# Kernel optimization log

Measured on AMD Instinct MI355X. Metric: run time of the kernel, lower is better.

The kernel has to match this reference:

```python
import jax, jax.numpy as jnp
import numpy as np

MAX_SAMPLE = 1024
THRESHOLD = 100
FEAT_W = 0.1
MASK_W = 0.1
TEMP = 0.1
BASE_TEMP = 0.07
IGNORE = 255
EPS = 1e-16


def _l2norm(x, axis):
    # F.normalize: x / max(||x||, 1e-12)
    return x / jnp.maximum(jnp.linalg.norm(x, axis=axis, keepdims=True), 1e-12)


def _mine(predict, label, prob):
    """Host-side hard-sample mining (data-dependent shapes, matches torch loop).
    predict, label: np [B,N]; prob: np [B,N,cls]. Returns (batch_idx, pixel_idx) or None."""
    B = label.shape[0]
    cls_lists, total = [], 0
    for i in range(B):
        vals, counts = np.unique(label[i], return_counts=True)
        per = [int(v) for v, c in zip(vals, counts) if v != IGNORE and c > THRESHOLD]
        cls_lists.append(per)
        total += len(per)
    if total == 0:
        return None
    n_view = min(MAX_SAMPLE // total, THRESHOLD)
    b_list, p_list = [], []
    for i in range(B):
        for c in cls_lists[i]:
            is_c = label[i] == c
            hard = np.nonzero(is_c & (predict[i] != c))[0]
            easy = np.nonzero(is_c & (predict[i] == c))[0]
            nh, ne = hard.shape[0], easy.shape[0]
            if nh >= n_view / 2 and ne >= n_view / 2:
                nhk = n_view // 2
                nek = n_view - nhk
            elif nh >= n_view / 2:
                nek = ne
                nhk = n_view - nek
            elif ne >= n_view / 2:
                nhk = nh
                nek = n_view - nhk
            else:
                nhk = nh
                nek = ne
            hard = hard[np.argsort(-prob[i, hard, c])[:nhk]]  # descending by prob
            easy = easy[np.argsort(prob[i, easy, c])[:nek]]   # ascending by prob
            idx = np.concatenate([hard, easy])
            b_list.append(np.full(idx.shape[0], i, dtype=np.int64))
            p_list.append(idx.astype(np.int64))
    return np.concatenate(b_list), np.concatenate(p_list)


def _feat_contrastive(feature, label):
    n = feature.shape[0]
    logits = feature @ feature.T / TEMP                              # [n,n]
    logits = logits - jax.lax.stop_gradient(jnp.max(logits, axis=1, keepdims=True))
    off_diag = ~jnp.eye(n, dtype=bool)
    pos = ((label[:, None] == label[None, :]) & off_diag).astype(logits.dtype)
    exp_logits = jnp.exp(logits) * off_diag
    log_prob = logits - jnp.log(exp_logits.sum(1, keepdims=True) + EPS)
    mlpp = (pos * log_prob).sum(1) / (pos.sum(1) + EPS)
    return (-(TEMP / BASE_TEMP) * mlpp).mean() * FEAT_W


def _mask_contrastive(anchors, keys, label):
    n, k, c = keys.shape
    all_keys = jnp.concatenate([anchors, keys.reshape(n * k, c)], axis=0)  # [n*(k+1),c]
    same = label[:, None] == label[None, :]
    key_label = jnp.tile(same, (1, k))  # matches torch .repeat(1, repeat_num)
    off_diag = ~jnp.eye(n, dtype=bool)
    tot = jnp.concatenate([same & off_diag, key_label], axis=1)
    neg = (~tot).astype(jnp.float32)
    tot = tot.astype(jnp.float32)
    logits = jnp.einsum('nc,mc->nm', jax.lax.stop_gradient(anchors), all_keys) / TEMP
    logits = logits - jax.lax.stop_gradient(jnp.max(logits, axis=1, keepdims=True))
    log_prob = logits - jnp.log((jnp.exp(logits) * neg).sum(1, keepdims=True) + EPS)
    mlp = (tot * log_prob).sum(1) / (tot.sum(1) + EPS)
    return (-(TEMP / BASE_TEMP) * mlp).mean() * MASK_W


def setup_inputs() -> dict:
    key = jax.random.key(0)
    k1, k2, k3, k4 = jax.random.split(key, 4)
    B, C, H, W = 2, 256, 160, 160
    NCLS, NM, CM = 19, 3, 256
    return {
        'proj_feats': jax.random.normal(k1, (B, C, H, W), jnp.float32),
        'seg_logits': jax.random.normal(k2, (B, NCLS, H, W), jnp.float32),
        'groundtruth': jax.random.randint(k3, (B, 1, H, W), 0, NCLS, dtype=jnp.int32),
        'proj_masks': jax.random.normal(k4, (NM, B, CM, H, W), jnp.float32),
    }


def reference(proj_feats, seg_logits, groundtruth, proj_masks):
    B, C, H, W = proj_feats.shape
    N = H * W
    # groundtruth already at [H,W] -> nearest interp is identity; bilinear same-size is identity.
    label = groundtruth.reshape(B, N)
    prob = jax.nn.softmax(seg_logits, axis=1).reshape(B, -1, N).transpose(0, 2, 1)  # [B,N,cls]
    predict = jnp.argmax(prob, axis=2)                                              # [B,N]
    feats = _l2norm(proj_feats.reshape(B, C, N), 1).transpose(0, 2, 1)              # [B,N,C]
    masks = _l2norm(proj_masks, 2).reshape(proj_masks.shape[0], B, -1, N).transpose(0, 1, 3, 2)  # [M,B,N,Cm]
    mined = _mine(np.asarray(predict), np.asarray(label), np.asarray(prob))
    if mined is None:
        return jnp.stack([proj_feats.mean() * 0, proj_masks.mean() * 0])
    b_idx, p_idx = mined
    sel_feat = feats[b_idx, p_idx]                           # [n,C]
    sel_label = label[b_idx, p_idx]                          # [n]
    sel_anchor = masks[-1][b_idx, p_idx]                     # [n,Cm]
    sel_keys = masks[:-1][:, b_idx, p_idx].transpose(1, 0, 2)  # [n,K,Cm]
    loss_feat = _feat_contrastive(sel_feat, sel_label)
    loss_mask = _mask_contrastive(sel_anchor, sel_keys, sel_label)
    return jnp.stack([loss_feat, loss_mask])
```

## Files before the change

kernel.cpp:

```cpp
#include <hip/hip_runtime.h>
#include <hip/hip_bf16.h>
#include <math.h>

#define B_ 2
#define NCLS_ 19
#define N_ 25600
#define C_ 256
#define MAXN_ 1024
#define THRESH_ 100
#define MAXSAMP_ 1024
#define NLIST_ (B_*NCLS_*2)
#define NHIST_ (B_*NCLS_)
#define NBLK_ 200
#define CAP_ 6144
#define CAPL_ 25600
#define NRF_ 32
#define NRM_ 96

typedef __attribute__((ext_vector_type(8))) short bf16x8;
typedef __attribute__((ext_vector_type(4))) float f32x4;

constexpr size_t OFF_CURS = 0;
constexpr size_t OFF_SELB = 512;
constexpr size_t OFF_SELP = OFF_SELB + (size_t)MAXN_*4;
constexpr size_t OFF_SELL = OFF_SELP + (size_t)MAXN_*4;
constexpr size_t OFF_SFH  = OFF_SELL + (size_t)MAXN_*4;
constexpr size_t OFF_KMH  = OFF_SFH + (size_t)MAXN_*C_*2;
constexpr size_t OFF_PAF  = OFF_KMH + (size_t)3*MAXN_*C_*2;
constexpr size_t OFF_PAM  = OFF_PAF + (size_t)MAXN_*4;
constexpr size_t OFF_PFP  = OFF_PAM + (size_t)MAXN_*4;
constexpr size_t OFF_PMP  = OFF_PFP + (size_t)MAXN_*NRF_*16;
constexpr size_t OFF_CAND = OFF_PMP + (size_t)MAXN_*NRM_*16;

__device__ __forceinline__ unsigned short f2bf(float x) {
    unsigned u = __float_as_uint(x);
    unsigned r = (u + 0x7FFFu + ((u >> 16) & 1u)) >> 16;
    return (unsigned short)r;
}

__device__ __forceinline__ void plan_takes(int ne, int nh, int n_view, int* h, int* e) {
    int nhk, nek;
    bool hb = 2*nh >= n_view, eb = 2*ne >= n_view;
    if (hb && eb)      { nhk = n_view/2; nek = n_view - nhk; }
    else if (hb)       { nek = ne;       nhk = n_view - nek; }
    else if (eb)       { nhk = nh;       nek = n_view - nhk; }
    else               { nhk = nh;       nek = ne; }
    *h = nhk < nh ? nhk : nh;
    *e = nek < ne ? nek : ne;
}

__device__ __forceinline__ int plan_total_n(const int* __restrict__ cursor, int* o_total) {
    int total = 0;
    for (int i = 0; i < NHIST_; ++i)
        if (cursor[2*i] + cursor[2*i+1] > THRESH_) total++;
    int n_view = 0;
    if (total > 0) { n_view = MAXSAMP_ / total; if (n_view > THRESH_) n_view = THRESH_; }
    int off = 0;
    for (int i = 0; i < NHIST_; ++i) {
        int ne = cursor[2*i], nh = cursor[2*i+1];
        if (ne + nh > THRESH_) { int h, e; plan_takes(ne, nh, n_view, &h, &e); off += h + e; }
    }
    if (o_total) *o_total = total;
    return off;
}

__device__ __forceinline__ void plan_slot(const int* __restrict__ cursor, int slot,
                                          int* h_take, int* e_take, int* off_out) {
    int total = 0;
    for (int i = 0; i < NHIST_; ++i)
        if (cursor[2*i] + cursor[2*i+1] > THRESH_) total++;
    int n_view = 0;
    if (total > 0) { n_view = MAXSAMP_ / total; if (n_view > THRESH_) n_view = THRESH_; }
    int off = 0, ht = 0, et = 0, myoff = 0;
    for (int i = 0; i < NHIST_; ++i) {
        int ne = cursor[2*i], nh = cursor[2*i+1];
        int h = 0, e = 0;
        if (ne + nh > THRESH_) plan_takes(ne, nh, n_view, &h, &e);
        if (i == slot) { ht = h; et = e; myoff = off; }
        off += h + e;
    }
    *h_take = ht; *e_take = et; *off_out = myoff;
}

__global__ void __launch_bounds__(256, 2)
k_softmax_scatter(const float* __restrict__ seg, const int* __restrict__ gt,
                  int* __restrict__ cursor, unsigned long long* __restrict__ cand) {
    __shared__ int lcnt[NLIST_];
    __shared__ int lbeg[NLIST_];
    int t = threadIdx.x;
    if (t < NLIST_) lcnt[t] = 0;
    __syncthreads();
    int idx = blockIdx.x * 256 + t;
    int L = -1, lp = 0;
    unsigned long long key = 0;
    if (idx < B_*N_) {
        int b = idx / N_, p = idx - b*N_;
        int lab = gt[idx];
        if (lab >= 0 && lab < NCLS_) {
            const float* base = seg + (size_t)b*NCLS_*N_ + p;
            float v[NCLS_];
            float mx = -INFINITY; int am = 0;
            #pragma unroll
            for (int k = 0; k < NCLS_; ++k) {
                float x = base[(size_t)k*N_];
                v[k] = x;
                if (x > mx) { mx = x; am = k; }
            }
            float ssum = 0.f, pv = 0.f;
            #pragma unroll
            for (int k = 0; k < NCLS_; ++k) {
                float e = expf(v[k] - mx);
                ssum += e;
                pv = (lab == k) ? e : pv;
            }
            pv /= ssum;
            int ishard = (am != lab) ? 1 : 0;
            L = (b*NCLS_ + lab)*2 + ishard;
            lp = atomicAdd(&lcnt[L], 1);
            unsigned int pb = __float_as_uint(pv);
            unsigned int lo = ishard ? (0xFFFFFFFFu - (unsigned int)p) : (unsigned int)p;
            key = ((unsigned long long)pb << 32) | (unsigned long long)lo;
        }
    }
    __syncthreads();
    if (t < NLIST_ && lcnt[t] > 0) lbeg[t] = atomicAdd(&cursor[t], lcnt[t]);
    __syncthreads();
    if (L >= 0) cand[(size_t)L*CAPL_ + lbeg[L] + lp] = key;
}

__global__ void __launch_bounds__(256, 2)
k_select2(const int* __restrict__ cursor, const unsigned long long* __restrict__ cand,
          int* __restrict__ sel_b, int* __restrict__ sel_p, int* __restrict__ sel_l) {
    __shared__ unsigned long long keys[CAP_];
    __shared__ unsigned long long wpart[2][4];
    int bid = blockIdx.x;
    int slot = bid >> 1, ishard = bid & 1;
    int h_take, e_take, base_off;
    plan_slot(cursor, slot, &h_take, &e_take, &base_off);
    int take = ishard ? h_take : e_take;
    if (take == 0) return;
    int off = base_off + (ishard ? 0 : h_take);
    int m = cursor[2*slot + ishard];
    const unsigned long long* g = cand + (size_t)(2*slot + ishard)*CAPL_;
    int t = threadIdx.x, lane = t & 63, w = t >> 6;
    bool fits = (m <= CAP_);
    if (fits) {
        for (int j = t; j < m; j += 256) keys[j] = g[j];
        __syncthreads();
    }
    int b = slot / NCLS_, c = slot - b*NCLS_;
    unsigned long long prev = ishard ? 0xFFFFFFFFFFFFFFFFull : 0ull;
    for (int it = 0; it < take; ++it) {
        unsigned long long best = ishard ? 0ull : 0xFFFFFFFFFFFFFFFFull;
        if (ishard) {
            for (int j = t; j < m; j += 256) {
                unsigned long long k = fits ? keys[j] : g[j];
                if (k < prev && k > best) best = k;
            }
        } else {
            for (int j = t; j < m; j += 256) {
                unsigned long long k = fits ? keys[j] : g[j];
                if (k > prev && k < best) best = k;
            }
        }
        #pragma unroll
        for (int d = 1; d < 64; d <<= 1) {
            unsigned long long o = __shfl_xor(best, d);
            if (ishard ? (o > best) : (o < best)) best = o;
        }
        if (lane == 0) wpart[it & 1][w] = best;
        __syncthreads();
        unsigned long long b0 = wpart[it & 1][0], b1 = wpart[it & 1][1];
        unsigned long long b2 = wpart[it & 1][2], b3 = wpart[it & 1][3];
        if (ishard) {
            unsigned long long hi01 = b0 > b1 ? b0 : b1;
            unsigned long long hi23 = b2 > b3 ? b2 : b3;
            prev = hi01 > hi23 ? hi01 : hi23;
        } else {
            unsigned long long lo01 = b0 < b1 ? b0 : b1;
            unsigned long long lo23 = b2 < b3 ? b2 : b3;
            prev = lo01 < lo23 ? lo01 : lo23;
        }
        if (t == 0) {
            unsigned int lo = (unsigned int)(prev & 0xFFFFFFFFull);
            int p = ishard ? (int)(0xFFFFFFFFu - lo) : (int)lo;
            sel_b[off+it] = b; sel_p[off+it] = p; sel_l[off+it] = c;
        }
    }
}

__global__ void __launch_bounds__(64)
k_gather(const float* __restrict__ pf, const float* __restrict__ pm,
         const int* __restrict__ cursor, const int* __restrict__ sel_b,
         const int* __restrict__ sel_p,
         unsigned short* __restrict__ sfh, unsigned short* __restrict__ km) {
    int bid = blockIdx.x;
    int s = bid >> 2, vec = bid & 3;
    int n = plan_total_n(cursor, nullptr);
    if (s >= n) return;
    int b = sel_b[s], p = sel_p[s];
    int lane = threadIdx.x;
    const float* src;
    unsigned short* dst;
    if (vec == 0)      { src = pf + (size_t)(b*C_)*N_ + p;          dst = sfh + (size_t)s*C_; }
    else if (vec == 1) { src = pm + (size_t)((2*B_+b)*C_)*N_ + p;   dst = km + (size_t)s*C_; }
    else if (vec == 2) { src = pm + (size_t)((0*B_+b)*C_)*N_ + p;   dst = km + (size_t)(n + 2*s)*C_; }
    else               { src = pm + (size_t)((1*B_+b)*C_)*N_ + p;   dst = km + (size_t)(n + 2*s + 1)*C_; }
    float x[4]; float ss = 0.f;
    #pragma unroll
    for (int q = 0; q < 4; ++q) { x[q] = src[(size_t)(lane + 64*q)*N_]; ss += x[q]*x[q]; }
    #pragma unroll
    for (int d = 1; d < 64; d <<= 1) ss += __shfl_xor(ss, d);
    float inv = 1.f / fmaxf(sqrtf(ss), 1e-12f);
    #pragma unroll
    for (int q = 0; q < 4; ++q) dst[lane + 64*q] = f2bf(x[q] * inv);
}

__global__ void __launch_bounds__(256, 4)
k_rows_mfma(const int* __restrict__ cursor, const unsigned short* __restrict__ sfh,
            const unsigned short* __restrict__ km, const int* __restrict__ sel_l,
            float4* __restrict__ pfp, float4* __restrict__ pmp) {
    const int n = plan_total_n(cursor, nullptr);
    const bool maskmode = (blockIdx.y >= 16);
    const int yb = maskmode ? (blockIdx.y - 16) : blockIdx.y;
    const int M = maskmode ? 3*n : n;
    const int rbase = blockIdx.x * 64;
    const int cbase = yb * 64;
    if (rbase >= n || cbase >= M) return;
    const unsigned short* buf = maskmode ? km : sfh;
    float4* part = maskmode ? pmp : pfp;
    const int NR = maskmode ? NRM_ : NRF_;

    __shared__ int sl[MAXN_];
    const int t = threadIdx.x;
    for (int j = t; j < n; j += 256) sl[j] = sel_l[j];
    __syncthreads();

    const int wid = t >> 6, lane = t & 63;
    const int wr = wid >> 1, wc = wid & 1;
    const int r0 = rbase + wr*32;
    const int c0 = cbase + wc*32;
    const int lrow = lane & 15, lk = (lane >> 4) * 8;

    const bf16x8 zero8 = {0,0,0,0,0,0,0,0};
    f32x4 acc[2][2];
    #pragma unroll
    for (int i = 0; i < 2; ++i)
        #pragma unroll
        for (int j = 0; j < 2; ++j) acc[i][j] = (f32x4){0.f,0.f,0.f,0.f};

    for (int kk = 0; kk < C_; kk += 32) {
        bf16x8 af[2], bfr[2];
        #pragma unroll
        for (int i = 0; i < 2; ++i) {
            int r = r0 + i*16 + lrow;
            af[i] = (r < n) ? *(const bf16x8*)&buf[(size_t)r*C_ + kk + lk] : zero8;
        }
        #pragma unroll
        for (int j = 0; j < 2; ++j) {
            int c = c0 + j*16 + lrow;
            bfr[j] = (c < M) ? *(const bf16x8*)&buf[(size_t)c*C_ + kk + lk] : zero8;
        }
        #pragma unroll
        for (int i = 0; i < 2; ++i)
            #pragma unroll
            for (int j = 0; j < 2; ++j)
                acc[i][j] = __builtin_amdgcn_mfma_f32_16x16x32_bf16(af[i], bfr[j], acc[i][j], 0, 0, 0);
    }

    const int ri = yb*2 + wc;
    const int g4 = (lane >> 4) * 4;
    const int lc = lane & 15;
    #pragma unroll
    for (int i = 0; i < 2; ++i) {
        #pragma unroll
        for (int q = 0; q < 4; ++q) {
            int row = r0 + i*16 + g4 + q;
            bool rok = (row < n);
            int la = rok ? sl[row] : 0;
            float v0 = acc[i][0][q] * 10.0f;
            float v1 = acc[i][1][q] * 10.0f;
            int col0 = c0 + lc, col1 = c0 + 16 + lc;
            float m = -INFINITY;
            if (col0 < M) m = v0;
            if (col1 < M) m = fmaxf(m, v1);
            #pragma unroll
            for (int d = 1; d < 16; d <<= 1) m = fmaxf(m, __shfl_xor(m, d, 16));
            float dn = 0.f, S = 0.f, cnt = 0.f;
            #pragma unroll
            for (int jj = 0; jj < 2; ++jj) {
                int col = jj ? col1 : col0;
                float L = jj ? v1 : v0;
                if (col >= M) continue;
                if (!maskmode) {
                    if (col != row) {
                        dn += expf(L - m);
                        if (sl[col] == la) { S += L; cnt += 1.f; }
                    }
                } else {
                    int qq = col - n;
                    int qm = (col < n) ? col : (qq < n ? qq : qq - n);
                    bool tot = (sl[qm] == la) && (col >= n || col != row);
                    if (tot) { S += L; cnt += 1.f; }
                    else dn += expf(L - m);
                }
            }
            #pragma unroll
            for (int d = 1; d < 16; d <<= 1) {
                dn  += __shfl_xor(dn, d, 16);
                S   += __shfl_xor(S, d, 16);
                cnt += __shfl_xor(cnt, d, 16);
            }
            if (rok && lc == 0) part[(size_t)row*NR + ri] = make_float4(m, dn, S, cnt);
        }
    }
}

__global__ void __launch_bounds__(256, 2)
k_combine_final(const int* __restrict__ cursor, const float4* __restrict__ pfp,
                const float4* __restrict__ pmp, float* __restrict__ paf,
                float* __restrict__ pam, int* __restrict__ counter,
                float* __restrict__ out) {
    int total;
    int n = plan_total_n(cursor, &total);
    int t = threadIdx.x;
    int r = blockIdx.x*256 + t;
    if (r < n) {
        {
            int nr = (n + 31) >> 5;
            float mg = -INFINITY;
            for (int i = 0; i < nr; ++i) mg = fmaxf(mg, pfp[(size_t)r*NRF_ + i].x);
            float dn = 0.f, S = 0.f, cnt = 0.f;
            for (int i = 0; i < nr; ++i) {
                float4 p = pfp[(size_t)r*NRF_ + i];
                dn += p.y * expf(p.x - mg);
                S += p.z; cnt += p.w;
            }
            float lg = logf(dn + 1e-16f);
            paf[r] = (S - cnt*mg - cnt*lg) / (cnt + 1e-16f);
        }
        {
            int nr = (3*n + 31) >> 5;
            float mg = -INFINITY;
            for (int i = 0; i < nr; ++i) mg = fmaxf(mg, pmp[(size_t)r*NRM_ + i].x);
            float dn = 0.f, S = 0.f, cnt = 0.f;
            for (int i = 0; i < nr; ++i) {
                float4 p = pmp[(size_t)r*NRM_ + i];
                dn += p.y * expf(p.x - mg);
                S += p.z; cnt += p.w;
            }
            float lg = logf(dn + 1e-16f);
            pam[r] = (S - cnt*mg - cnt*lg) / (cnt + 1e-16f);
        }
    }
    __threadfence();
    __shared__ int amLast;
    if (t == 0) amLast = (atomicAdd(counter, 1) == (int)gridDim.x - 1);
    __syncthreads();
    if (!amLast) return;
    __threadfence();
    __shared__ float redf[4][2];
    int lane = t & 63, w = t >> 6;
    float sf = 0.f, sm = 0.f;
    for (int a = t; a < n; a += 256) { sf += paf[a]; sm += pam[a]; }
    #pragma unroll
    for (int d = 1; d < 64; d <<= 1) { sf += __shfl_xor(sf, d); sm += __shfl_xor(sm, d); }
    if (lane == 0) { redf[w][0] = sf; redf[w][1] = sm; }
    __syncthreads();
    if (t == 0) {
        sf = redf[0][0] + redf[1][0] + redf[2][0] + redf[3][0];
        sm = redf[0][1] + redf[1][1] + redf[2][1] + redf[3][1];
        if (total == 0 || n == 0) { out[0] = 0.f; out[1] = 0.f; }
        else {
            float scale = (float)(-(0.1/0.07));
            out[0] = scale * (sf / (float)n) * 0.1f;
            out[1] = scale * (sm / (float)n) * 0.1f;
        }
    }
}

extern "C" void kernel_launch(void* const* d_in, const int* in_sizes, int n_in,
                              void* d_out, int out_size, void* d_ws, size_t ws_size,
                              hipStream_t stream) {
    const float* pf  = (const float*)d_in[0];
    const float* seg = (const float*)d_in[1];
    const int*   gt  = (const int*)d_in[2];
    const float* pm  = (const float*)d_in[3];
    float* out = (float*)d_out;
    char* ws = (char*)d_ws;

    int*   cursor   = (int*)(ws + OFF_CURS);
    int*   counter  = cursor + NLIST_;
    int*   sel_b    = (int*)(ws + OFF_SELB);
    int*   sel_p    = (int*)(ws + OFF_SELP);
    int*   sel_l    = (int*)(ws + OFF_SELL);
    unsigned short* sfh = (unsigned short*)(ws + OFF_SFH);
    unsigned short* km  = (unsigned short*)(ws + OFF_KMH);
    float* paf      = (float*)(ws + OFF_PAF);
    float* pam      = (float*)(ws + OFF_PAM);
    float4* pfp     = (float4*)(ws + OFF_PFP);
    float4* pmp     = (float4*)(ws + OFF_PMP);
    unsigned long long* cand = (unsigned long long*)(ws + OFF_CAND);

    hipMemsetAsync(ws + OFF_CURS, 0, 512, stream);

    k_softmax_scatter<<<NBLK_, 256, 0, stream>>>(seg, gt, cursor, cand);
    k_select2<<<NLIST_, 256, 0, stream>>>(cursor, cand, sel_b, sel_p, sel_l);
    k_gather<<<4*MAXN_, 64, 0, stream>>>(pf, pm, cursor, sel_b, sel_p, sfh, km);
    k_rows_mfma<<<dim3(MAXN_/64, 64), 256, 0, stream>>>(cursor, sfh, km, sel_l, pfp, pmp);
    k_combine_final<<<(MAXN_ + 255)/256, 256, 0, stream>>>(cursor, pfp, pmp, paf, pam, counter, out);
}
```

Before: 132.1 us.

## Fuse row contrastive GEMM and combine into one full-row kernel

Replaces the tiled GEMM kernel plus partial-stat combine kernel with a single kernel where each block owns 16 rows and sweeps all columns, reducing in shared memory and writing the per-row loss directly. Because features are L2-normalised, the fixed upper bound 10 replaces the running row max, which removes the max pass and the partial buffers. This saves one launch and the partial-result round trip through memory. The cost is far fewer blocks (128), lower parallelism, and B-operand rows re-read from cache by every block.

```diff
diff --git a/kernel.cpp b/kernel.cpp
--- a/kernel.cpp
+++ b/kernel.cpp
@@ -14,8 +14,6 @@
 #define NBLK_ 200
 #define CAP_ 6144
 #define CAPL_ 25600
-#define NRF_ 32
-#define NRM_ 96
 
 typedef __attribute__((ext_vector_type(8))) short bf16x8;
 typedef __attribute__((ext_vector_type(4))) float f32x4;
@@ -28,9 +26,7 @@
 constexpr size_t OFF_KMH  = OFF_SFH + (size_t)MAXN_*C_*2;
 constexpr size_t OFF_PAF  = OFF_KMH + (size_t)3*MAXN_*C_*2;
 constexpr size_t OFF_PAM  = OFF_PAF + (size_t)MAXN_*4;
-constexpr size_t OFF_PFP  = OFF_PAM + (size_t)MAXN_*4;
-constexpr size_t OFF_PMP  = OFF_PFP + (size_t)MAXN_*NRF_*16;
-constexpr size_t OFF_CAND = OFF_PMP + (size_t)MAXN_*NRM_*16;
+constexpr size_t OFF_CAND = OFF_PAM + (size_t)MAXN_*4;
 
 __device__ __forceinline__ unsigned short f2bf(float x) {
     unsigned u = __float_as_uint(x);
@@ -216,146 +212,106 @@
     for (int q = 0; q < 4; ++q) dst[lane + 64*q] = f2bf(x[q] * inv);
 }
 
-__global__ void __launch_bounds__(256, 4)
-k_rows_mfma(const int* __restrict__ cursor, const unsigned short* __restrict__ sfh,
+__global__ void __launch_bounds__(256, 2)
+k_rows_full(const int* __restrict__ cursor, const unsigned short* __restrict__ sfh,
             const unsigned short* __restrict__ km, const int* __restrict__ sel_l,
-            float4* __restrict__ pfp, float4* __restrict__ pmp) {
-    const int n = plan_total_n(cursor, nullptr);
-    const bool maskmode = (blockIdx.y >= 16);
-    const int yb = maskmode ? (blockIdx.y - 16) : blockIdx.y;
-    const int M = maskmode ? 3*n : n;
-    const int rbase = blockIdx.x * 64;
-    const int cbase = yb * 64;
-    if (rbase >= n || cbase >= M) return;
-    const unsigned short* buf = maskmode ? km : sfh;
-    float4* part = maskmode ? pmp : pfp;
-    const int NR = maskmode ? NRM_ : NRF_;
-
+            float* __restrict__ paf, float* __restrict__ pam,
+            int* __restrict__ counter, float* __restrict__ out) {
+    int total;
+    const int n = plan_total_n(cursor, &total);
+    const int t = threadIdx.x;
+    const bool maskmode = (blockIdx.x >= 64);
+    const int r0 = (maskmode ? (int)blockIdx.x - 64 : (int)blockIdx.x) * 16;
     __shared__ int sl[MAXN_];
-    const int t = threadIdx.x;
-    for (int j = t; j < n; j += 256) sl[j] = sel_l[j];
-    __syncthreads();
-
-    const int wid = t >> 6, lane = t & 63;
-    const int wr = wid >> 1, wc = wid & 1;
-    const int r0 = rbase + wr*32;
-    const int c0 = cbase + wc*32;
-    const int lrow = lane & 15, lk = (lane >> 4) * 8;
-
-    const bf16x8 zero8 = {0,0,0,0,0,0,0,0};
-    f32x4 acc[2][2];
-    #pragma unroll
-    for (int i = 0; i < 2; ++i)
+    __shared__ float red[16][3];
+    const bool active = (n > 0) && (r0 < n);
+    if (active) {
+        for (int j = t; j < n; j += 256) sl[j] = sel_l[j];
+        if (t < 16) { red[t][0] = 0.f; red[t][1] = 0.f; red[t][2] = 0.f; }
+        __syncthreads();
+        const unsigned short* buf = maskmode ? km : sfh;
+        const int M = maskmode ? 3*n : n;
+        const int w = t >> 6, lane = t & 63;
+        const int lrow = lane & 15, koff = (lane >> 4) * 8;
+        const bf16x8 zero8 = {0,0,0,0,0,0,0,0};
+        bf16x8 af[8];
+        const int arow = r0 + lrow;
+        const bool aok = (arow < n);
         #pragma unroll
-        for (int j = 0; j < 2; ++j) acc[i][j] = (f32x4){0.f,0.f,0.f,0.f};
-
-    for (int kk = 0; kk < C_; kk += 32) {
-        bf16x8 af[2], bfr[2];
-        #pragma unroll
-        for (int i = 0; i < 2; ++i) {
-            int r = r0 + i*16 + lrow;
-            af[i] = (r < n) ? *(const bf16x8*)&buf[(size_t)r*C_ + kk + lk] : zero8;
-        }
-        #pragma unroll
-        for (int j = 0; j < 2; ++j) {
-            int c = c0 + j*16 + lrow;
-            bfr[j] = (c < M) ? *(const bf16x8*)&buf[(size_t)c*C_ + kk + lk] : zero8;
-        }
-        #pragma unroll
-        for (int i = 0; i < 2; ++i)
-            #pragma unroll
-            for (int j = 0; j < 2; ++j)
-                acc[i][j] = __builtin_amdgcn_mfma_f32_16x16x32_bf16(af[i], bfr[j], acc[i][j], 0, 0, 0);
-    }
-
-    const int ri = yb*2 + wc;
-    const int g4 = (lane >> 4) * 4;
-    const int lc = lane & 15;
-    #pragma unroll
-    for (int i = 0; i < 2; ++i) {
+        for (int ch = 0; ch < 8; ++ch)
+            af[ch] = aok ? *(const bf16x8*)&buf[(size_t)arow*C_ + ch*32 + koff] : zero8;
+        int rowq[4], laq[4]; bool rokq[4];
         #pragma unroll
         for (int q = 0; q < 4; ++q) {
-            int row = r0 + i*16 + g4 + q;
-            bool rok = (row < n);
-            int la = rok ? sl[row] : 0;
-            float v0 = acc[i][0][q] * 10.0f;
-            float v1 = acc[i][1][q] * 10.0f;
-            int col0 = c0 + lc, col1 = c0 + 16 + lc;
-            float m = -INFINITY;
-            if (col0 < M) m = v0;
-            if (col1 < M) m = fmaxf(m, v1);
-            #pragma unroll
-            for (int d = 1; d < 16; d <<= 1) m = fmaxf(m, __shfl_xor(m, d, 16));
-            float dn = 0.f, S = 0.f, cnt = 0.f;
-            #pragma unroll
-            for (int jj = 0; jj < 2; ++jj) {
-                int col = jj ? col1 : col0;
-                float L = jj ? v1 : v0;
-                if (col >= M) continue;
+            rowq[q] = r0 + ((lane >> 4) << 2) + q;
+            rokq[q] = rowq[q] < n;
+            laq[q] = rokq[q] ? sl[rowq[q]] : -1;
+        }
+        float dn[4] = {0,0,0,0}, S[4] = {0,0,0,0}, cnt[4] = {0,0,0,0};
+        const int ncg = (M + 15) >> 4;
+        for (int cg = w; cg < ncg; cg += 4) {
+            const int bcol = cg*16 + lrow;
+            const bool bok = (bcol < M);
+            const unsigned short* bsrc = buf + (size_t)bcol*C_ + koff;
+            f32x4 acc = (f32x4){0.f,0.f,0.f,0.f};
+            #pragma unroll
+            for (int ch = 0; ch < 8; ++ch) {
+                bf16x8 bfr = bok ? *(const bf16x8*)&bsrc[ch*32] : zero8;
+                acc = __builtin_amdgcn_mfma_f32_16x16x32_bf16(af[ch], bfr, acc, 0, 0, 0);
+            }
+            const int col = cg*16 + lrow;
+            const bool colok = (col < M);
+            int lcl = -1;
+            if (colok) {
+                int qm = col;
+                if (maskmode) { int qq = col - n; qm = (col < n) ? col : (qq < n ? qq : qq - n); }
+                lcl = sl[qm];
+            }
+            #pragma unroll
+            for (int q = 0; q < 4; ++q) {
+                if (!colok || !rokq[q]) continue;
+                float Lv = acc[q] * 10.0f;
                 if (!maskmode) {
-                    if (col != row) {
-                        dn += expf(L - m);
-                        if (sl[col] == la) { S += L; cnt += 1.f; }
+                    if (col != rowq[q]) {
+                        dn[q] += expf(Lv - 10.0f);
+                        if (lcl == laq[q]) { S[q] += Lv; cnt[q] += 1.f; }
                     }
                 } else {
-                    int qq = col - n;
-                    int qm = (col < n) ? col : (qq < n ? qq : qq - n);
-                    bool tot = (sl[qm] == la) && (col >= n || col != row);
-                    if (tot) { S += L; cnt += 1.f; }
-                    else dn += expf(L - m);
+                    bool tot = (lcl == laq[q]) && (col >= n || col != rowq[q]);
+                    if (tot) { S[q] += Lv; cnt[q] += 1.f; }
+                    else dn[q] += expf(Lv - 10.0f);
                 }
             }
-            #pragma unroll
-            for (int d = 1; d < 16; d <<= 1) {
-                dn  += __shfl_xor(dn, d, 16);
-                S   += __shfl_xor(S, d, 16);
-                cnt += __shfl_xor(cnt, d, 16);
-            }
-            if (rok && lc == 0) part[(size_t)row*NR + ri] = make_float4(m, dn, S, cnt);
-        }
-    }
-}
-
-__global__ void __launch_bounds__(256, 2)
-k_combine_final(const int* __restrict__ cursor, const float4* __restrict__ pfp,
-                const float4* __restrict__ pmp, float* __restrict__ paf,
-                float* __restrict__ pam, int* __restrict__ counter,
-                float* __restrict__ out) {
-    int total;
-    int n = plan_total_n(cursor, &total);
-    int t = threadIdx.x;
-    int r = blockIdx.x*256 + t;
-    if (r < n) {
-        {
-            int nr = (n + 31) >> 5;
-            float mg = -INFINITY;
-            for (int i = 0; i < nr; ++i) mg = fmaxf(mg, pfp[(size_t)r*NRF_ + i].x);
-            float dn = 0.f, S = 0.f, cnt = 0.f;
-            for (int i = 0; i < nr; ++i) {
-                float4 p = pfp[(size_t)r*NRF_ + i];
-                dn += p.y * expf(p.x - mg);
-                S += p.z; cnt += p.w;
-            }
-            float lg = logf(dn + 1e-16f);
-            paf[r] = (S - cnt*mg - cnt*lg) / (cnt + 1e-16f);
-        }
-        {
-            int nr = (3*n + 31) >> 5;
-            float mg = -INFINITY;
-            for (int i = 0; i < nr; ++i) mg = fmaxf(mg, pmp[(size_t)r*NRM_ + i].x);
-            float dn = 0.f, S = 0.f, cnt = 0.f;
-            for (int i = 0; i < nr; ++i) {
-                float4 p = pmp[(size_t)r*NRM_ + i];
-                dn += p.y * expf(p.x - mg);
-                S += p.z; cnt += p.w;
-            }
-            float lg = logf(dn + 1e-16f);
-            pam[r] = (S - cnt*mg - cnt*lg) / (cnt + 1e-16f);
+        }
+        #pragma unroll
+        for (int d = 1; d < 16; d <<= 1) {
+            #pragma unroll
+            for (int q = 0; q < 4; ++q) {
+                dn[q]  += __shfl_xor(dn[q], d, 16);
+                S[q]   += __shfl_xor(S[q], d, 16);
+                cnt[q] += __shfl_xor(cnt[q], d, 16);
+            }
+        }
+        if (lrow == 0) {
+            #pragma unroll
+            for (int q = 0; q < 4; ++q) {
+                int rl = ((lane >> 4) << 2) + q;
+                atomicAdd(&red[rl][0], dn[q]);
+                atomicAdd(&red[rl][1], S[q]);
+                atomicAdd(&red[rl][2], cnt[q]);
+            }
+        }
+        __syncthreads();
+        if (t < 16 && (r0 + t) < n) {
+            float d = red[t][0], s = red[t][1], c = red[t][2];
+            float lg = logf(d + 1e-16f);
+            float val = (s - c*10.0f - c*lg) / (c + 1e-16f);
+            (maskmode ? pam : paf)[r0 + t] = val;
         }
     }
     __threadfence();
     __shared__ int amLast;
-    if (t == 0) amLast = (atomicAdd(counter, 1) == (int)gridDim.x - 1);
+    if (t == 0) amLast = (atomicAdd(counter, 1) == 127);
     __syncthreads();
     if (!amLast) return;
     __threadfence();
@@ -398,8 +354,6 @@
     unsigned short* km  = (unsigned short*)(ws + OFF_KMH);
     float* paf      = (float*)(ws + OFF_PAF);
     float* pam      = (float*)(ws + OFF_PAM);
-    float4* pfp     = (float4*)(ws + OFF_PFP);
-    float4* pmp     = (float4*)(ws + OFF_PMP);
     unsigned long long* cand = (unsigned long long*)(ws + OFF_CAND);
 
     hipMemsetAsync(ws + OFF_CURS, 0, 512, stream);
@@ -407,6 +361,5 @@
     k_softmax_scatter<<<NBLK_, 256, 0, stream>>>(seg, gt, cursor, cand);
     k_select2<<<NLIST_, 256, 0, stream>>>(cursor, cand, sel_b, sel_p, sel_l);
     k_gather<<<4*MAXN_, 64, 0, stream>>>(pf, pm, cursor, sel_b, sel_p, sfh, km);
-    k_rows_mfma<<<dim3(MAXN_/64, 64), 256, 0, stream>>>(cursor, sfh, km, sel_l, pfp, pmp);
-    k_combine_final<<<(MAXN_ + 255)/256, 256, 0, stream>>>(cursor, pfp, pmp, paf, pam, counter, out);
-}
+    k_rows_full<<<128, 256, 0, stream>>>(cursor, sfh, km, sel_l, paf, pam, counter, out);
+}
```

Result: slower. 183.0 us (+38.5%).

## Fuse gather into selection and combine into MFMA rows kernel

Applied to the files above, without the earlier changes.

Merges the row gather and normalisation into the top-k selection kernel, so each selection block gathers the rows it picked, using one wave per feature or mask source. It also folds the combine step into the MFMA rows kernel: per-row partial sums go to a global accumulator via atomics, and a last-block finalisation produces the output. Since the vectors are L2-normalised, the per-tile row max is replaced by the constant bound 10. This removes two kernel launches and the partial-buffer round trip. In exchange, the gather now runs serially over each block's picks in only 76 blocks, and it adds atomic contention and a hardcoded grid count of 1023 in the last-block check.

```diff
diff --git a/kernel.cpp b/kernel.cpp
--- a/kernel.cpp
+++ b/kernel.cpp
@@ -14,23 +14,16 @@
 #define NBLK_ 200
 #define CAP_ 6144
 #define CAPL_ 25600
-#define NRF_ 32
-#define NRM_ 96
 
 typedef __attribute__((ext_vector_type(8))) short bf16x8;
 typedef __attribute__((ext_vector_type(4))) float f32x4;
 
-constexpr size_t OFF_CURS = 0;
-constexpr size_t OFF_SELB = 512;
-constexpr size_t OFF_SELP = OFF_SELB + (size_t)MAXN_*4;
-constexpr size_t OFF_SELL = OFF_SELP + (size_t)MAXN_*4;
-constexpr size_t OFF_SFH  = OFF_SELL + (size_t)MAXN_*4;
-constexpr size_t OFF_KMH  = OFF_SFH + (size_t)MAXN_*C_*2;
-constexpr size_t OFF_PAF  = OFF_KMH + (size_t)3*MAXN_*C_*2;
-constexpr size_t OFF_PAM  = OFF_PAF + (size_t)MAXN_*4;
-constexpr size_t OFF_PFP  = OFF_PAM + (size_t)MAXN_*4;
-constexpr size_t OFF_PMP  = OFF_PFP + (size_t)MAXN_*NRF_*16;
-constexpr size_t OFF_CAND = OFF_PMP + (size_t)MAXN_*NRM_*16;
+constexpr size_t OFF_ACC   = 512;
+constexpr size_t ZERO_BYTES = 512 + (size_t)6*MAXN_*4;
+constexpr size_t OFF_SELL  = ZERO_BYTES;
+constexpr size_t OFF_SFH   = OFF_SELL + (size_t)MAXN_*4;
+constexpr size_t OFF_KMH   = OFF_SFH + (size_t)MAXN_*C_*2;
+constexpr size_t OFF_CAND  = OFF_KMH + (size_t)3*MAXN_*C_*2;
 
 __device__ __forceinline__ unsigned short f2bf(float x) {
     unsigned u = __float_as_uint(x);
@@ -51,11 +44,13 @@
 
 __device__ __forceinline__ int plan_total_n(const int* __restrict__ cursor, int* o_total) {
     int total = 0;
+    #pragma unroll
     for (int i = 0; i < NHIST_; ++i)
         if (cursor[2*i] + cursor[2*i+1] > THRESH_) total++;
     int n_view = 0;
     if (total > 0) { n_view = MAXSAMP_ / total; if (n_view > THRESH_) n_view = THRESH_; }
     int off = 0;
+    #pragma unroll
     for (int i = 0; i < NHIST_; ++i) {
         int ne = cursor[2*i], nh = cursor[2*i+1];
         if (ne + nh > THRESH_) { int h, e; plan_takes(ne, nh, n_view, &h, &e); off += h + e; }
@@ -64,14 +59,16 @@
     return off;
 }
 
-__device__ __forceinline__ void plan_slot(const int* __restrict__ cursor, int slot,
-                                          int* h_take, int* e_take, int* off_out) {
+__device__ __forceinline__ void plan_slot2(const int* __restrict__ cursor, int slot,
+                                           int* h_take, int* e_take, int* off_out, int* n_out) {
     int total = 0;
+    #pragma unroll
     for (int i = 0; i < NHIST_; ++i)
         if (cursor[2*i] + cursor[2*i+1] > THRESH_) total++;
     int n_view = 0;
     if (total > 0) { n_view = MAXSAMP_ / total; if (n_view > THRESH_) n_view = THRESH_; }
     int off = 0, ht = 0, et = 0, myoff = 0;
+    #pragma unroll
     for (int i = 0; i < NHIST_; ++i) {
         int ne = cursor[2*i], nh = cursor[2*i+1];
         int h = 0, e = 0;
@@ -79,7 +76,7 @@
         if (i == slot) { ht = h; et = e; myoff = off; }
         off += h + e;
     }
-    *h_take = ht; *e_take = et; *off_out = myoff;
+    *h_take = ht; *e_take = et; *off_out = myoff; *n_out = off;
 }
 
 __global__ void __launch_bounds__(256, 2)
@@ -129,14 +126,17 @@
 }
 
 __global__ void __launch_bounds__(256, 2)
-k_select2(const int* __restrict__ cursor, const unsigned long long* __restrict__ cand,
-          int* __restrict__ sel_b, int* __restrict__ sel_p, int* __restrict__ sel_l) {
+k_select_gather(const int* __restrict__ cursor, const unsigned long long* __restrict__ cand,
+                const float* __restrict__ pf, const float* __restrict__ pm,
+                int* __restrict__ sel_l, unsigned short* __restrict__ sfh,
+                unsigned short* __restrict__ km) {
     __shared__ unsigned long long keys[CAP_];
     __shared__ unsigned long long wpart[2][4];
+    __shared__ int pickP[112];
     int bid = blockIdx.x;
     int slot = bid >> 1, ishard = bid & 1;
-    int h_take, e_take, base_off;
-    plan_slot(cursor, slot, &h_take, &e_take, &base_off);
+    int h_take, e_take, base_off, nall;
+    plan_slot2(cursor, slot, &h_take, &e_take, &base_off, &nall);
     int take = ishard ? h_take : e_take;
     if (take == 0) return;
     int off = base_off + (ishard ? 0 : h_take);
@@ -184,185 +184,143 @@
         if (t == 0) {
             unsigned int lo = (unsigned int)(prev & 0xFFFFFFFFull);
             int p = ishard ? (int)(0xFFFFFFFFu - lo) : (int)lo;
-            sel_b[off+it] = b; sel_p[off+it] = p; sel_l[off+it] = c;
-        }
-    }
-}
-
-__global__ void __launch_bounds__(64)
-k_gather(const float* __restrict__ pf, const float* __restrict__ pm,
-         const int* __restrict__ cursor, const int* __restrict__ sel_b,
-         const int* __restrict__ sel_p,
-         unsigned short* __restrict__ sfh, unsigned short* __restrict__ km) {
-    int bid = blockIdx.x;
-    int s = bid >> 2, vec = bid & 3;
-    int n = plan_total_n(cursor, nullptr);
-    if (s >= n) return;
-    int b = sel_b[s], p = sel_p[s];
-    int lane = threadIdx.x;
-    const float* src;
-    unsigned short* dst;
-    if (vec == 0)      { src = pf + (size_t)(b*C_)*N_ + p;          dst = sfh + (size_t)s*C_; }
-    else if (vec == 1) { src = pm + (size_t)((2*B_+b)*C_)*N_ + p;   dst = km + (size_t)s*C_; }
-    else if (vec == 2) { src = pm + (size_t)((0*B_+b)*C_)*N_ + p;   dst = km + (size_t)(n + 2*s)*C_; }
-    else               { src = pm + (size_t)((1*B_+b)*C_)*N_ + p;   dst = km + (size_t)(n + 2*s + 1)*C_; }
-    float x[4]; float ss = 0.f;
-    #pragma unroll
-    for (int q = 0; q < 4; ++q) { x[q] = src[(size_t)(lane + 64*q)*N_]; ss += x[q]*x[q]; }
-    #pragma unroll
-    for (int d = 1; d < 64; d <<= 1) ss += __shfl_xor(ss, d);
-    float inv = 1.f / fmaxf(sqrtf(ss), 1e-12f);
-    #pragma unroll
-    for (int q = 0; q < 4; ++q) dst[lane + 64*q] = f2bf(x[q] * inv);
+            sel_l[off+it] = c;
+            pickP[it] = p;
+        }
+        __syncthreads();
+    }
+    const float* srcb;
+    if (w == 0)      srcb = pf + (size_t)(b*C_)*N_;
+    else if (w == 1) srcb = pm + (size_t)((2*B_ + b)*C_)*N_;
+    else if (w == 2) srcb = pm + (size_t)((0*B_ + b)*C_)*N_;
+    else             srcb = pm + (size_t)((1*B_ + b)*C_)*N_;
+    for (int it = 0; it < take; ++it) {
+        int p = pickP[it];
+        int s = off + it;
+        unsigned short* dst;
+        if (w == 0)      dst = sfh + (size_t)s*C_;
+        else if (w == 1) dst = km + (size_t)s*C_;
+        else if (w == 2) dst = km + (size_t)(nall + 2*s)*C_;
+        else             dst = km + (size_t)(nall + 2*s + 1)*C_;
+        const float* src = srcb + p;
+        float x[4]; float ss = 0.f;
+        #pragma unroll
+        for (int q = 0; q < 4; ++q) { x[q] = src[(size_t)(lane + 64*q)*N_]; ss += x[q]*x[q]; }
+        #pragma unroll
+        for (int d = 1; d < 64; d <<= 1) ss += __shfl_xor(ss, d);
+        float inv = 1.f / fmaxf(sqrtf(ss), 1e-12f);
+        #pragma unroll
+        for (int q = 0; q < 4; ++q) dst[lane + 64*q] = f2bf(x[q] * inv);
+    }
 }
 
 __global__ void __launch_bounds__(256, 4)
-k_rows_mfma(const int* __restrict__ cursor, const unsigned short* __restrict__ sfh,
-            const unsigned short* __restrict__ km, const int* __restrict__ sel_l,
-            float4* __restrict__ pfp, float4* __restrict__ pmp) {
-    const int n = plan_total_n(cursor, nullptr);
+k_rows_final(const int* __restrict__ cursor, const unsigned short* __restrict__ sfh,
+             const unsigned short* __restrict__ km, const int* __restrict__ sel_l,
+             float* __restrict__ acc, int* __restrict__ counter, float* __restrict__ out) {
+    int total;
+    const int n = plan_total_n(cursor, &total);
+    const int t = threadIdx.x;
     const bool maskmode = (blockIdx.y >= 16);
     const int yb = maskmode ? (blockIdx.y - 16) : blockIdx.y;
     const int M = maskmode ? 3*n : n;
     const int rbase = blockIdx.x * 64;
     const int cbase = yb * 64;
-    if (rbase >= n || cbase >= M) return;
-    const unsigned short* buf = maskmode ? km : sfh;
-    float4* part = maskmode ? pmp : pfp;
-    const int NR = maskmode ? NRM_ : NRF_;
-
-    __shared__ int sl[MAXN_];
-    const int t = threadIdx.x;
-    for (int j = t; j < n; j += 256) sl[j] = sel_l[j];
-    __syncthreads();
-
-    const int wid = t >> 6, lane = t & 63;
-    const int wr = wid >> 1, wc = wid & 1;
-    const int r0 = rbase + wr*32;
-    const int c0 = cbase + wc*32;
-    const int lrow = lane & 15, lk = (lane >> 4) * 8;
-
-    const bf16x8 zero8 = {0,0,0,0,0,0,0,0};
-    f32x4 acc[2][2];
-    #pragma unroll
-    for (int i = 0; i < 2; ++i)
-        #pragma unroll
-        for (int j = 0; j < 2; ++j) acc[i][j] = (f32x4){0.f,0.f,0.f,0.f};
-
-    for (int kk = 0; kk < C_; kk += 32) {
-        bf16x8 af[2], bfr[2];
+    const bool active = (n > 0) && (rbase < n) && (cbase < M);
+    if (active) {
+        const unsigned short* buf = maskmode ? km : sfh;
+        float* a0 = acc + (maskmode ? 3 : 0)*MAXN_;
+        __shared__ int sl[MAXN_];
+        for (int j = t; j < n; j += 256) sl[j] = sel_l[j];
+        __syncthreads();
+
+        const int wid = t >> 6, lane = t & 63;
+        const int wr = wid >> 1, wc = wid & 1;
+        const int r0 = rbase + wr*32;
+        const int c0 = cbase + wc*32;
+        const int lrow = lane & 15, lk = (lane >> 4) * 8;
+
+        const bf16x8 zero8 = {0,0,0,0,0,0,0,0};
+        f32x4 a00 = (f32x4){0.f,0.f,0.f,0.f}, a01 = a00, a10 = a00, a11 = a00;
+
+        for (int kk = 0; kk < C_; kk += 32) {
+            bf16x8 af0, af1, bf0, bf1;
+            {
+                int r = r0 + lrow;
+                af0 = (r < n) ? *(const bf16x8*)&buf[(size_t)r*C_ + kk + lk] : zero8;
+                r = r0 + 16 + lrow;
+                af1 = (r < n) ? *(const bf16x8*)&buf[(size_t)r*C_ + kk + lk] : zero8;
+                int c = c0 + lrow;
+                bf0 = (c < M) ? *(const bf16x8*)&buf[(size_t)c*C_ + kk + lk] : zero8;
+                c = c0 + 16 + lrow;
+                bf1 = (c < M) ? *(const bf16x8*)&buf[(size_t)c*C_ + kk + lk] : zero8;
+            }
+            a00 = __builtin_amdgcn_mfma_f32_16x16x32_bf16(af0, bf0, a00, 0, 0, 0);
+            a01 = __builtin_amdgcn_mfma_f32_16x16x32_bf16(af0, bf1, a01, 0, 0, 0);
+            a10 = __builtin_amdgcn_mfma_f32_16x16x32_bf16(af1, bf0, a10, 0, 0, 0);
+            a11 = __builtin_amdgcn_mfma_f32_16x16x32_bf16(af1, bf1, a11, 0, 0, 0);
+        }
+
+        const int g4 = (lane >> 4) * 4;
+        const int lc = lane & 15;
         #pragma unroll
         for (int i = 0; i < 2; ++i) {
-            int r = r0 + i*16 + lrow;
-            af[i] = (r < n) ? *(const bf16x8*)&buf[(size_t)r*C_ + kk + lk] : zero8;
-        }
-        #pragma unroll
-        for (int j = 0; j < 2; ++j) {
-            int c = c0 + j*16 + lrow;
-            bfr[j] = (c < M) ? *(const bf16x8*)&buf[(size_t)c*C_ + kk + lk] : zero8;
-        }
-        #pragma unroll
-        for (int i = 0; i < 2; ++i)
             #pragma unroll
-            for (int j = 0; j < 2; ++j)
-                acc[i][j] = __builtin_amdgcn_mfma_f32_16x16x32_bf16(af[i], bfr[j], acc[i][j], 0, 0, 0);
-    }
-
-    const int ri = yb*2 + wc;
-    const int g4 = (lane >> 4) * 4;
-    const int lc = lane & 15;
-    #pragma unroll
-    for (int i = 0; i < 2; ++i) {
-        #pragma unroll
-        for (int q = 0; q < 4; ++q) {
-            int row = r0 + i*16 + g4 + q;
-            bool rok = (row < n);
-            int la = rok ? sl[row] : 0;
-            float v0 = acc[i][0][q] * 10.0f;
-            float v1 = acc[i][1][q] * 10.0f;
-            int col0 = c0 + lc, col1 = c0 + 16 + lc;
-            float m = -INFINITY;
-            if (col0 < M) m = v0;
-            if (col1 < M) m = fmaxf(m, v1);
-            #pragma unroll
-            for (int d = 1; d < 16; d <<= 1) m = fmaxf(m, __shfl_xor(m, d, 16));
-            float dn = 0.f, S = 0.f, cnt = 0.f;
-            #pragma unroll
-            for (int jj = 0; jj < 2; ++jj) {
-                int col = jj ? col1 : col0;
-                float L = jj ? v1 : v0;
-                if (col >= M) continue;
-                if (!maskmode) {
-                    if (col != row) {
-                        dn += expf(L - m);
-                        if (sl[col] == la) { S += L; cnt += 1.f; }
+            for (int q = 0; q < 4; ++q) {
+                int row = r0 + i*16 + g4 + q;
+                bool rok = (row < n);
+                int la = rok ? sl[row] : -1;
+                float v0 = (i ? a10[q] : a00[q]) * 10.0f;
+                float v1 = (i ? a11[q] : a01[q]) * 10.0f;
+                int col0 = c0 + lc, col1 = c0 + 16 + lc;
+                float dn = 0.f, S = 0.f, cnt = 0.f;
+                #pragma unroll
+                for (int jj = 0; jj < 2; ++jj) {
+                    int col = jj ? col1 : col0;
+                    float L = jj ? v1 : v0;
+                    if (col >= M || !rok) continue;
+                    if (!maskmode) {
+                        if (col != row) {
+                            dn += expf(L - 10.0f);
+                            if (sl[col] == la) { S += L; cnt += 1.f; }
+                        }
+                    } else {
+                        int qq = col - n;
+                        int qm = (col < n) ? col : (qq < n ? qq : qq - n);
+                        bool tot = (sl[qm] == la) && (col >= n || col != row);
+                        if (tot) { S += L; cnt += 1.f; }
+                        else dn += expf(L - 10.0f);
                     }
-                } else {
-                    int qq = col - n;
-                    int qm = (col < n) ? col : (qq < n ? qq : qq - n);
-                    bool tot = (sl[qm] == la) && (col >= n || col != row);
-                    if (tot) { S += L; cnt += 1.f; }
-                    else dn += expf(L - m);
                 }
-            }
-            #pragma unroll
-            for (int d = 1; d < 16; d <<= 1) {
-                dn  += __shfl_xor(dn, d, 16);
-                S   += __shfl_xor(S, d, 16);
-                cnt += __shfl_xor(cnt, d, 16);
-            }
-            if (rok && lc == 0) part[(size_t)row*NR + ri] = make_float4(m, dn, S, cnt);
-        }
-    }
-}
-
-__global__ void __launch_bounds__(256, 2)
-k_combine_final(const int* __restrict__ cursor, const float4* __restrict__ pfp,
-                const float4* __restrict__ pmp, float* __restrict__ paf,
-                float* __restrict__ pam, int* __restrict__ counter,
-                float* __restrict__ out) {
-    int total;
-    int n = plan_total_n(cursor, &total);
-    int t = threadIdx.x;
-    int r = blockIdx.x*256 + t;
-    if (r < n) {
-        {
-            int nr = (n + 31) >> 5;
-            float mg = -INFINITY;
-            for (int i = 0; i < nr; ++i) mg = fmaxf(mg, pfp[(size_t)r*NRF_ + i].x);
-            float dn = 0.f, S = 0.f, cnt = 0.f;
-            for (int i = 0; i < nr; ++i) {
-                float4 p = pfp[(size_t)r*NRF_ + i];
-                dn += p.y * expf(p.x - mg);
-                S += p.z; cnt += p.w;
-            }
-            float lg = logf(dn + 1e-16f);
-            paf[r] = (S - cnt*mg - cnt*lg) / (cnt + 1e-16f);
-        }
-        {
-            int nr = (3*n + 31) >> 5;
-            float mg = -INFINITY;
-            for (int i = 0; i < nr; ++i) mg = fmaxf(mg, pmp[(size_t)r*NRM_ + i].x);
-            float dn = 0.f, S = 0.f, cnt = 0.f;
-            for (int i = 0; i < nr; ++i) {
-                float4 p = pmp[(size_t)r*NRM_ + i];
-                dn += p.y * expf(p.x - mg);
-                S += p.z; cnt += p.w;
-            }
-            float lg = logf(dn + 1e-16f);
-            pam[r] = (S - cnt*mg - cnt*lg) / (cnt + 1e-16f);
+                #pragma unroll
+                for (int d = 1; d < 16; d <<= 1) {
+                    dn  += __shfl_xor(dn, d, 16);
+                    S   += __shfl_xor(S, d, 16);
+                    cnt += __shfl_xor(cnt, d, 16);
+                }
+                if (rok && lc == 0) {
+                    atomicAdd(&a0[row], dn);
+                    atomicAdd(&a0[MAXN_ + row], S);
+                    atomicAdd(&a0[2*MAXN_ + row], cnt);
+                }
+            }
         }
     }
     __threadfence();
     __shared__ int amLast;
-    if (t == 0) amLast = (atomicAdd(counter, 1) == (int)gridDim.x - 1);
+    if (t == 0) amLast = (atomicAdd(counter, 1) == 1023);
     __syncthreads();
     if (!amLast) return;
     __threadfence();
     __shared__ float redf[4][2];
     int lane = t & 63, w = t >> 6;
     float sf = 0.f, sm = 0.f;
-    for (int a = t; a < n; a += 256) { sf += paf[a]; sm += pam[a]; }
+    for (int a = t; a < n; a += 256) {
+        float d = acc[a], s = acc[MAXN_ + a], c = acc[2*MAXN_ + a];
+        sf += (s - c*10.0f - c*logf(d + 1e-16f)) / (c + 1e-16f);
+        d = acc[3*MAXN_ + a]; s = acc[4*MAXN_ + a]; c = acc[5*MAXN_ + a];
+        sm += (s - c*10.0f - c*logf(d + 1e-16f)) / (c + 1e-16f);
+    }
     #pragma unroll
     for (int d = 1; d < 64; d <<= 1) { sf += __shfl_xor(sf, d); sm += __shfl_xor(sm, d); }
     if (lane == 0) { redf[w][0] = sf; redf[w][1] = sm; }
@@ -389,24 +347,17 @@
     float* out = (float*)d_out;
     char* ws = (char*)d_ws;
 
-    int*   cursor   = (int*)(ws + OFF_CURS);
+    int*   cursor   = (int*)ws;
     int*   counter  = cursor + NLIST_;
-    int*   sel_b    = (int*)(ws + OFF_SELB);
-    int*   sel_p    = (int*)(ws + OFF_SELP);
+    float* acc      = (float*)(ws + OFF_ACC);
     int*   sel_l    = (int*)(ws + OFF_SELL);
     unsigned short* sfh = (unsigned short*)(ws + OFF_SFH);
     unsigned short* km  = (unsigned short*)(ws + OFF_KMH);
-    float* paf      = (float*)(ws + OFF_PAF);
-    float* pam      = (float*)(ws + OFF_PAM);
-    float4* pfp     = (float4*)(ws + OFF_PFP);
-    float4* pmp     = (float4*)(ws + OFF_PMP);
     unsigned long long* cand = (unsigned long long*)(ws + OFF_CAND);
 
-    hipMemsetAsync(ws + OFF_CURS, 0, 512, stream);
+    hipMemsetAsync(ws, 0, ZERO_BYTES, stream);
 
     k_softmax_scatter<<<NBLK_, 256, 0, stream>>>(seg, gt, cursor, cand);
-    k_select2<<<NLIST_, 256, 0, stream>>>(cursor, cand, sel_b, sel_p, sel_l);
-    k_gather<<<4*MAXN_, 64, 0, stream>>>(pf, pm, cursor, sel_b, sel_p, sfh, km);
-    k_rows_mfma<<<dim3(MAXN_/64, 64), 256, 0, stream>>>(cursor, sfh, km, sel_l, pfp, pmp);
-    k_combine_final<<<(MAXN_ + 255)/256, 256, 0, stream>>>(cursor, pfp, pmp, paf, pam, counter, out);
-}
+    k_select_gather<<<NLIST_, 256, 0, stream>>>(cursor, cand, pf, pm, sel_l, sfh, km);
+    k_rows_final<<<dim3(16, 64), 256, 0, stream>>>(cursor, sfh, km, sel_l, acc, counter, out);
+}
```

After: 161.3 us. +22.1%, slower.
